# Kernel tuning notes

Hardware: AMD Instinct MI355X
Metric: run time of the kernel (lower is better)

The kernel has to match this reference:

```python
import jax, jax.numpy as jnp
import numpy as np

LOG_STD_MAX = 2.0
LOG_STD_MIN = -5.0
N_LAYERS = 10
HID = 512
OBS = 21
ACT = 8
OVERALL = HID * (N_LAYERS + 1)          # 5632
IN_DIM = OBS + OVERALL                   # 5653
OUT_DIM = OVERALL + ACT                  # 5640
BATCH = 8192


def _block_banded_weight(rng):
    # staircase partitions, exactly as layer_init
    in_d = [0, OBS] + [OBS + HID * i for i in range(1, N_LAYERS + 2)]
    out_d = [0] + [HID * i for i in range(1, N_LAYERS + 2)] + [OUT_DIM]
    W = np.zeros((OUT_DIM, IN_DIM), dtype=np.float32)
    for i in range(N_LAYERS + 2):
        r0, r1 = out_d[i], out_d[i + 1]
        c0, c1 = in_d[i], in_d[i + 1]
        fan_in = c1 - c0
        std = np.sqrt(2.0 / fan_in)  # kaiming_normal_ fan_in, gain sqrt(2)
        W[r0:r1, c0:c1] = rng.standard_normal((r1 - r0, c1 - c0)).astype(np.float32) * std
    return jnp.asarray(W)


def setup_inputs() -> dict:
    key = jax.random.key(0)
    k1, k2, k3, k4, k5, k6 = jax.random.split(key, 6)
    rng = np.random.default_rng(0)
    return {
        "obs": jax.random.normal(k1, (BATCH, OBS), dtype=jnp.float32),
        "hidden0": jax.random.uniform(k2, (BATCH, OVERALL), dtype=jnp.float32),
        "prev_mean": jax.random.normal(k3, (BATCH, ACT), dtype=jnp.float32),
        "prev_logstd": jax.random.normal(k4, (BATCH, ACT), dtype=jnp.float32),
        "W_mean": _block_banded_weight(rng),
        "b_mean": jnp.zeros((OUT_DIM,), dtype=jnp.float32),
        "W_logstd": jax.random.normal(k5, (ACT, IN_DIM), dtype=jnp.float32) / np.sqrt(IN_DIM),
        "b_logstd": jax.random.normal(k6, (ACT,), dtype=jnp.float32) * 0.01,
    }


def reference(obs, hidden0, prev_mean, prev_logstd, W_mean, b_mean, W_logstd, b_logstd):
    x = jnp.concatenate([obs, hidden0], axis=1)            # [B, IN_DIM]
    new_x = x @ W_mean.T + b_mean                          # [B, OUT_DIM]
    new_hidden = jax.nn.relu(new_x[:, :-ACT])              # [B, OVERALL]
    new_mean = new_x[:, -ACT:]                             # [B, ACT]
    new_log_std = x @ W_logstd.T + b_logstd                # [B, ACT]
    # outputs come from the PREVIOUS step's (mean, log_std)
    log_std = jnp.tanh(prev_logstd)
    log_std = LOG_STD_MIN + 0.5 * (LOG_STD_MAX - LOG_STD_MIN) * (log_std + 1.0)
    return (prev_mean, log_std, new_hidden, new_mean, new_log_std)
```

## Files before the change

### kernel.cpp

```cpp
#include <hip/hip_runtime.h>
#include <math.h>

typedef unsigned short u16;
typedef unsigned int u32;
typedef __attribute__((ext_vector_type(8))) short short8;
typedef __attribute__((ext_vector_type(4))) float float4v;

#define BATCH   8192
#define OBS     21
#define HID     512
#define NL      10
#define OVERALL 5632
#define IN_DIM  5653
#define ACT     8

#define O_PM   0
#define O_LS   65536
#define O_NH   131072
#define O_NM   (131072 + BATCH*OVERALL)
#define O_NLS  (O_NM + 65536)

#define WSP_TOTAL (10*512*512)
#define WSP_BYTES ((size_t)WSP_TOTAL * 2)

__device__ __forceinline__ u16 f2bf(float f) {
    u32 u = __float_as_uint(f);
    u32 r = (u + 0x7fffu + ((u >> 16) & 1u)) >> 16;
    return (u16)r;
}
__device__ __forceinline__ u32 pkbf(float a, float b) {
    return (u32)f2bf(a) | ((u32)f2bf(b) << 16);
}
__device__ __forceinline__ void gload_lds16(const void* g, void* l) {
    __builtin_amdgcn_global_load_lds(
        (const __attribute__((address_space(1))) char*)g,
        (__attribute__((address_space(3))) char*)l, 16, 0, 0);
}

__global__ __launch_bounds__(256) void k_pack(const float* __restrict__ Wm,
                                              u16* __restrict__ ws) {
    int idx4 = blockIdx.x * 256 + threadIdx.x;
    if (idx4 >= WSP_TOTAL / 4) return;
    int idx = idx4 * 4;
    int z = idx >> 18;
    int rem = idx & 262143;
    int n = rem >> 9, k = rem & 511;
    const float* g = Wm + (size_t)(512 * (z + 1) + n) * IN_DIM + OBS + 512 * z + k;
    ushort4 o;
    o.x = f2bf(g[0]); o.y = f2bf(g[1]); o.z = f2bf(g[2]); o.w = f2bf(g[3]);
    *(ushort4*)&ws[idx] = o;
}

#define BM 128
#define BK 32
#define LDA 40
__global__ __launch_bounds__(1024, 4) void k_fused(
        const float* __restrict__ X,
        const float* __restrict__ Wm_raw,
        const u16* __restrict__ Wp,
        const float* __restrict__ Wls_raw,
        const float* __restrict__ b_mean,
        float* __restrict__ out_h,
        float* __restrict__ out_ls,
        float* __restrict__ out_mean,
        int packed) {
    __shared__ __attribute__((aligned(16))) u16 As[BM * LDA];
    __shared__ __attribute__((aligned(16))) u16 Bs[512 * 32];
    __shared__ __attribute__((aligned(16))) u16 Wt[16 * 520];
    u16* Wt2 = (u16*)Bs;

    int t = threadIdx.x;
    int w = t >> 6, lane = t & 63;
    int quad = lane >> 4, r16 = lane & 15;
    int gm = blockIdx.x * BM;
    int z = blockIdx.y;
    bool mainz = (z < 10);
    int wm = (w >> 3) * 64;
    int wn = (w & 7) * 64;

    {
        int n = t >> 7;
        int k4 = (t & 127) * 4;
        const float* wr = Wls_raw + (size_t)n * IN_DIM + OBS + z * 512 + k4;
        u16* dst = &Wt[n * 520 + k4];
        dst[0] = f2bf(wr[0]); dst[1] = f2bf(wr[1]);
        dst[2] = f2bf(wr[2]); dst[3] = f2bf(wr[3]);
        if (!mainz) {
            const float* wr2 = Wm_raw + (size_t)(OVERALL + n) * IN_DIM + OBS + z * 512 + k4;
            u16* d2 = &Wt2[n * 520 + k4];
            d2[0] = f2bf(wr2[0]); d2[1] = f2bf(wr2[1]);
            d2[2] = f2bf(wr2[2]); d2[3] = f2bf(wr2[3]);
        }
    }

    int arow = t >> 3;
    int acol = (t & 7) * 4;
    const float* gA = X + (size_t)(gm + arow) * OVERALL + (size_t)z * 512 + acol;
    float4 areg = *(const float4*)(gA);

    float4v acc[4][4];
#pragma unroll
    for (int i = 0; i < 4; i++)
#pragma unroll
        for (int j = 0; j < 4; j++) acc[i][j] = (float4v)0.f;
    float4v accL = (float4v)0.f;

    for (int it = 0; it < 16; ++it) {
        int k0 = it * BK;
        __syncthreads();
        {
            uint2 p;
            p.x = pkbf(areg.x, areg.y);
            p.y = pkbf(areg.z, areg.w);
            *(uint2*)&As[arow * LDA + acol] = p;
        }
        if (mainz) {
            if (packed) {
#pragma unroll
                for (int i2 = 0; i2 < 2; ++i2) {
                    int base_row = i2 * 256 + w * 16;
                    int row = base_row + (lane >> 2);
                    int slot = lane & 3;
                    int j = (slot - row) & 3;
                    const u16* g = Wp + (size_t)z * 262144 + (size_t)row * 512 + k0 + j * 8;
                    gload_lds16(g, (char*)Bs + base_row * 64);
                }
            } else {
#pragma unroll
                for (int i2 = 0; i2 < 2; ++i2) {
                    int row = i2 * 256 + w * 16 + (lane >> 2);
                    int slot = lane & 3;
                    int j = (slot - row) & 3;
                    const float* g = Wm_raw + (size_t)(512 * (z + 1) + row) * IN_DIM
                                     + OBS + (size_t)z * 512 + k0 + j * 8;
                    uint4 q;
                    q.x = pkbf(g[0], g[1]); q.y = pkbf(g[2], g[3]);
                    q.z = pkbf(g[4], g[5]); q.w = pkbf(g[6], g[7]);
                    *(uint4*)&Bs[row * 32 + slot * 8] = q;
                }
            }
        }
        __syncthreads();
        if (it < 15) areg = *(const float4*)(gA + (it + 1) * BK);

        if (mainz) {
            short8 bfr[4];
#pragma unroll
            for (int j = 0; j < 4; j++) {
                int n = wn + j * 16 + r16;
                int s = (quad + n) & 3;
                bfr[j] = *(const short8*)&Bs[n * 32 + s * 8];
            }
#pragma unroll
            for (int i2 = 0; i2 < 4; i2++) {
                short8 af = *(const short8*)&As[(wm + i2 * 16 + r16) * LDA + quad * 8];
#pragma unroll
                for (int j = 0; j < 4; j++)
                    acc[i2][j] = __builtin_amdgcn_mfma_f32_16x16x32_bf16(af, bfr[j], acc[i2][j], 0, 0, 0);
            }
        }
        if (w < 8) {
            short8 aL = *(const short8*)&As[(w * 16 + r16) * LDA + quad * 8];
            short8 bL = *(const short8*)&Wt[r16 * 520 + k0 + quad * 8];
            accL = __builtin_amdgcn_mfma_f32_16x16x32_bf16(aL, bL, accL, 0, 0, 0);
        } else if (!mainz) {
            short8 aL = *(const short8*)&As[((w - 8) * 16 + r16) * LDA + quad * 8];
            short8 bL = *(const short8*)&Wt2[r16 * 520 + k0 + quad * 8];
            accL = __builtin_amdgcn_mfma_f32_16x16x32_bf16(aL, bL, accL, 0, 0, 0);
        }
    }

    if (mainz) {
        int colblock = (z + 1) * 512;
#pragma unroll
        for (int j = 0; j < 4; j++) {
            int n_loc = wn + j * 16 + r16;
            float bias = b_mean[colblock + n_loc];
#pragma unroll
            for (int i2 = 0; i2 < 4; i2++) {
                int m0 = gm + wm + i2 * 16 + quad * 4;
#pragma unroll
                for (int r = 0; r < 4; r++) {
                    float v = acc[i2][j][r] + bias;
                    out_h[(size_t)(m0 + r) * OVERALL + colblock + n_loc] = fmaxf(v, 0.f);
                }
            }
        }
    }
    if (w < 8) {
        if (r16 < ACT) {
#pragma unroll
            for (int r = 0; r < 4; r++) {
                int row = gm + w * 16 + quad * 4 + r;
                atomicAdd(&out_ls[(size_t)row * ACT + r16], accL[r]);
            }
        }
    } else if (!mainz) {
        if (r16 < ACT) {
            float bias = b_mean[OVERALL + r16];
#pragma unroll
            for (int r = 0; r < 4; r++) {
                int row = gm + (w - 8) * 16 + quad * 4 + r;
                out_mean[(size_t)row * ACT + r16] = accL[r] + bias;
            }
        }
    }
}

#define B0_ROWS 32
__global__ __launch_bounds__(256) void k_epi(const float* __restrict__ obs,
                                             const float* __restrict__ Wm,
                                             const float* __restrict__ b_mean,
                                             const float* __restrict__ Wls,
                                             const float* __restrict__ b_logstd,
                                             const float* __restrict__ pm,
                                             const float* __restrict__ pls,
                                             float* __restrict__ out_h,
                                             float* __restrict__ o_pm,
                                             float* __restrict__ o_lstd,
                                             float* __restrict__ o_nls) {
    __shared__ float w0[OBS * 512];
    __shared__ float bias_s[512];
    __shared__ float obs_s[B0_ROWS * OBS];
    __shared__ float wobs[ACT * OBS];
    __shared__ float bls_s[ACT];
    int t = threadIdx.x;
    int b0 = blockIdx.x * B0_ROWS;
    for (int i = t; i < OBS * 512; i += 256) {
        int n = i / OBS, k = i - n * OBS;
        w0[k * 512 + n] = Wm[(size_t)n * IN_DIM + k];
    }
    for (int i = t; i < 512; i += 256) bias_s[i] = b_mean[i];
    for (int i = t; i < B0_ROWS * OBS; i += 256) obs_s[i] = obs[(size_t)b0 * OBS + i];
    if (t < ACT * OBS) wobs[t] = Wls[(size_t)(t / OBS) * IN_DIM + (t % OBS)];
    if (t < ACT) bls_s[t] = b_logstd[t];
    __syncthreads();

    {
        int n0 = (t & 127) * 4;
        int rh = t >> 7;
#pragma unroll 4
        for (int r = 0; r < 16; r++) {
            int row = rh * 16 + r;
            float acc0 = bias_s[n0], acc1 = bias_s[n0 + 1];
            float acc2 = bias_s[n0 + 2], acc3 = bias_s[n0 + 3];
#pragma unroll
            for (int k = 0; k < OBS; k++) {
                float xo = obs_s[row * OBS + k];
                const float* wr = &w0[k * 512 + n0];
                acc0 += xo * wr[0]; acc1 += xo * wr[1];
                acc2 += xo * wr[2]; acc3 += xo * wr[3];
            }
            float4 o;
            o.x = fmaxf(acc0, 0.f); o.y = fmaxf(acc1, 0.f);
            o.z = fmaxf(acc2, 0.f); o.w = fmaxf(acc3, 0.f);
            *(float4*)&out_h[(size_t)(b0 + row) * OVERALL + n0] = o;
        }
    }

    {
        int rl = t >> 3;
        int n = t & 7;
        int row = b0 + rl;
        float a = bls_s[n];
#pragma unroll
        for (int k = 0; k < OBS; k++) a += obs_s[rl * OBS + k] * wobs[n * OBS + k];
        size_t off = (size_t)row * ACT + n;
        o_nls[off] += a;
        o_pm[off] = pm[off];
        float l = pls[off];
        o_lstd[off] = -5.f + 3.5f * (tanhf(l) + 1.f);
    }
}

extern "C" void kernel_launch(void* const* d_in, const int* in_sizes, int n_in,
                              void* d_out, int out_size, void* d_ws, size_t ws_size,
                              hipStream_t stream) {
    const float* obs         = (const float*)d_in[0];
    const float* hidden0     = (const float*)d_in[1];
    const float* prev_mean   = (const float*)d_in[2];
    const float* prev_logstd = (const float*)d_in[3];
    const float* W_mean      = (const float*)d_in[4];
    const float* b_mean      = (const float*)d_in[5];
    const float* W_logstd    = (const float*)d_in[6];
    const float* b_logstd    = (const float*)d_in[7];

    float* out   = (float*)d_out;
    float* o_pm  = out + O_PM;
    float* o_ls  = out + O_LS;
    float* o_nh  = out + O_NH;
    float* o_nm  = out + O_NM;
    float* o_nls = out + O_NLS;
    u16*   ws    = (u16*)d_ws;

    int packed = (ws != nullptr && ws_size >= WSP_BYTES) ? 1 : 0;

    if (packed) {
        k_pack<<<(WSP_TOTAL / 4 + 255) / 256, 256, 0, stream>>>(W_mean, ws);
    }
    hipMemsetAsync(o_nls, 0, (size_t)BATCH * ACT * sizeof(float), stream);
    k_fused<<<dim3(BATCH / BM, NL + 1), 1024, 0, stream>>>(
        hidden0, W_mean, ws, W_logstd, b_mean, o_nh, o_nls, o_nm, packed);
    k_epi<<<BATCH / B0_ROWS, 256, 0, stream>>>(obs, W_mean, b_mean,
                                               W_logstd, b_logstd,
                                               prev_mean, prev_logstd,
                                               o_nh, o_pm, o_ls, o_nls);
}
```

Baseline: 447.4 us.

## Make fused GEMM kernel persistent over 256 blocks with custom barriers

```diff
diff --git a/kernel.cpp b/kernel.cpp
--- a/kernel.cpp
+++ b/kernel.cpp
@@ -35,6 +35,14 @@
     __builtin_amdgcn_global_load_lds(
         (const __attribute__((address_space(1))) char*)g,
         (__attribute__((address_space(3))) char*)l, 16, 0, 0);
+}
+__device__ __forceinline__ void bar_lds() {
+    asm volatile("s_waitcnt lgkmcnt(0)" ::: "memory");
+    __builtin_amdgcn_s_barrier();
+}
+__device__ __forceinline__ void bar_full() {
+    asm volatile("s_waitcnt vmcnt(0) lgkmcnt(0)" ::: "memory");
+    __builtin_amdgcn_s_barrier();
 }
 
 __global__ __launch_bounds__(256) void k_pack(const float* __restrict__ Wm,
@@ -54,6 +62,7 @@
 #define BM 128
 #define BK 32
 #define LDA 40
+#define NTILES (64 * (NL + 1))
 __global__ __launch_bounds__(1024, 4) void k_fused(
         const float* __restrict__ X,
         const float* __restrict__ Wm_raw,
@@ -69,139 +78,145 @@
     __shared__ __attribute__((aligned(16))) u16 Wt[16 * 520];
     u16* Wt2 = (u16*)Bs;
 
-    int t = threadIdx.x;
-    int w = t >> 6, lane = t & 63;
-    int quad = lane >> 4, r16 = lane & 15;
-    int gm = blockIdx.x * BM;
-    int z = blockIdx.y;
-    bool mainz = (z < 10);
-    int wm = (w >> 3) * 64;
-    int wn = (w & 7) * 64;
-
-    {
-        int n = t >> 7;
-        int k4 = (t & 127) * 4;
-        const float* wr = Wls_raw + (size_t)n * IN_DIM + OBS + z * 512 + k4;
-        u16* dst = &Wt[n * 520 + k4];
-        dst[0] = f2bf(wr[0]); dst[1] = f2bf(wr[1]);
-        dst[2] = f2bf(wr[2]); dst[3] = f2bf(wr[3]);
-        if (!mainz) {
-            const float* wr2 = Wm_raw + (size_t)(OVERALL + n) * IN_DIM + OBS + z * 512 + k4;
-            u16* d2 = &Wt2[n * 520 + k4];
-            d2[0] = f2bf(wr2[0]); d2[1] = f2bf(wr2[1]);
-            d2[2] = f2bf(wr2[2]); d2[3] = f2bf(wr2[3]);
-        }
-    }
-
-    int arow = t >> 3;
-    int acol = (t & 7) * 4;
-    const float* gA = X + (size_t)(gm + arow) * OVERALL + (size_t)z * 512 + acol;
-    float4 areg = *(const float4*)(gA);
-
-    float4v acc[4][4];
-#pragma unroll
-    for (int i = 0; i < 4; i++)
-#pragma unroll
-        for (int j = 0; j < 4; j++) acc[i][j] = (float4v)0.f;
-    float4v accL = (float4v)0.f;
-
-    for (int it = 0; it < 16; ++it) {
-        int k0 = it * BK;
-        __syncthreads();
+    const int t = threadIdx.x;
+    const int w = t >> 6, lane = t & 63;
+    const int quad = lane >> 4, r16 = lane & 15;
+    const int wm = (w >> 3) * 64;
+    const int wn = (w & 7) * 64;
+    const int arow = t >> 3;
+    const int acol = (t & 7) * 4;
+
+#pragma unroll 1
+    for (int tile = blockIdx.x; tile < NTILES; tile += 256) {
+        const int gm = (tile & 63) * BM;
+        const int z = tile >> 6;
+        const bool mainz = (z < 10);
+
+        bar_lds();
+
         {
-            uint2 p;
-            p.x = pkbf(areg.x, areg.y);
-            p.y = pkbf(areg.z, areg.w);
-            *(uint2*)&As[arow * LDA + acol] = p;
-        }
+            int n = t >> 7;
+            int k4 = (t & 127) * 4;
+            const float* wr = Wls_raw + (size_t)n * IN_DIM + OBS + z * 512 + k4;
+            u16* dst = &Wt[n * 520 + k4];
+            dst[0] = f2bf(wr[0]); dst[1] = f2bf(wr[1]);
+            dst[2] = f2bf(wr[2]); dst[3] = f2bf(wr[3]);
+            if (!mainz) {
+                const float* wr2 = Wm_raw + (size_t)(OVERALL + n) * IN_DIM + OBS + z * 512 + k4;
+                u16* d2 = &Wt2[n * 520 + k4];
+                d2[0] = f2bf(wr2[0]); d2[1] = f2bf(wr2[1]);
+                d2[2] = f2bf(wr2[2]); d2[3] = f2bf(wr2[3]);
+            }
+        }
+
+        const float* gA = X + (size_t)(gm + arow) * OVERALL + (size_t)z * 512 + acol;
+        float4 areg = *(const float4*)(gA);
+
+        float4v acc[4][4];
+#pragma unroll
+        for (int i = 0; i < 4; i++)
+#pragma unroll
+            for (int j = 0; j < 4; j++) acc[i][j] = (float4v)0.f;
+        float4v accL = (float4v)0.f;
+
+        for (int it = 0; it < 16; ++it) {
+            int k0 = it * BK;
+            bar_lds();
+            {
+                uint2 p;
+                p.x = pkbf(areg.x, areg.y);
+                p.y = pkbf(areg.z, areg.w);
+                *(uint2*)&As[arow * LDA + acol] = p;
+            }
+            if (mainz) {
+                if (packed) {
+#pragma unroll
+                    for (int i2 = 0; i2 < 2; ++i2) {
+                        int base_row = i2 * 256 + w * 16;
+                        int row = base_row + (lane >> 2);
+                        int slot = lane & 3;
+                        int j = (slot - row) & 3;
+                        const u16* g = Wp + (size_t)z * 262144 + (size_t)row * 512 + k0 + j * 8;
+                        gload_lds16(g, (char*)Bs + base_row * 64);
+                    }
+                } else {
+#pragma unroll
+                    for (int i2 = 0; i2 < 2; ++i2) {
+                        int row = i2 * 256 + w * 16 + (lane >> 2);
+                        int slot = lane & 3;
+                        int j = (slot - row) & 3;
+                        const float* g = Wm_raw + (size_t)(512 * (z + 1) + row) * IN_DIM
+                                         + OBS + (size_t)z * 512 + k0 + j * 8;
+                        uint4 q;
+                        q.x = pkbf(g[0], g[1]); q.y = pkbf(g[2], g[3]);
+                        q.z = pkbf(g[4], g[5]); q.w = pkbf(g[6], g[7]);
+                        *(uint4*)&Bs[row * 32 + slot * 8] = q;
+                    }
+                }
+            }
+            bar_full();
+            if (it < 15) areg = *(const float4*)(gA + (it + 1) * BK);
+
+            if (mainz) {
+                short8 bfr[4];
+#pragma unroll
+                for (int j = 0; j < 4; j++) {
+                    int n = wn + j * 16 + r16;
+                    int s = (quad + n) & 3;
+                    bfr[j] = *(const short8*)&Bs[n * 32 + s * 8];
+                }
+#pragma unroll
+                for (int i2 = 0; i2 < 4; i2++) {
+                    short8 af = *(const short8*)&As[(wm + i2 * 16 + r16) * LDA + quad * 8];
+#pragma unroll
+                    for (int j = 0; j < 4; j++)
+                        acc[i2][j] = __builtin_amdgcn_mfma_f32_16x16x32_bf16(af, bfr[j], acc[i2][j], 0, 0, 0);
+                }
+            }
+            if (w < 8) {
+                short8 aL = *(const short8*)&As[(w * 16 + r16) * LDA + quad * 8];
+                short8 bL = *(const short8*)&Wt[r16 * 520 + k0 + quad * 8];
+                accL = __builtin_amdgcn_mfma_f32_16x16x32_bf16(aL, bL, accL, 0, 0, 0);
+            } else if (!mainz) {
+                short8 aL = *(const short8*)&As[((w - 8) * 16 + r16) * LDA + quad * 8];
+                short8 bL = *(const short8*)&Wt2[r16 * 520 + k0 + quad * 8];
+                accL = __builtin_amdgcn_mfma_f32_16x16x32_bf16(aL, bL, accL, 0, 0, 0);
+            }
+        }
+
         if (mainz) {
-            if (packed) {
-#pragma unroll
-                for (int i2 = 0; i2 < 2; ++i2) {
-                    int base_row = i2 * 256 + w * 16;
-                    int row = base_row + (lane >> 2);
-                    int slot = lane & 3;
-                    int j = (slot - row) & 3;
-                    const u16* g = Wp + (size_t)z * 262144 + (size_t)row * 512 + k0 + j * 8;
-                    gload_lds16(g, (char*)Bs + base_row * 64);
-                }
-            } else {
-#pragma unroll
-                for (int i2 = 0; i2 < 2; ++i2) {
-                    int row = i2 * 256 + w * 16 + (lane >> 2);
-                    int slot = lane & 3;
-                    int j = (slot - row) & 3;
-                    const float* g = Wm_raw + (size_t)(512 * (z + 1) + row) * IN_DIM
-                                     + OBS + (size_t)z * 512 + k0 + j * 8;
-                    uint4 q;
-                    q.x = pkbf(g[0], g[1]); q.y = pkbf(g[2], g[3]);
-                    q.z = pkbf(g[4], g[5]); q.w = pkbf(g[6], g[7]);
-                    *(uint4*)&Bs[row * 32 + slot * 8] = q;
-                }
-            }
-        }
-        __syncthreads();
-        if (it < 15) areg = *(const float4*)(gA + (it + 1) * BK);
-
-        if (mainz) {
-            short8 bfr[4];
+            int colblock = (z + 1) * 512;
 #pragma unroll
             for (int j = 0; j < 4; j++) {
-                int n = wn + j * 16 + r16;
-                int s = (quad + n) & 3;
-                bfr[j] = *(const short8*)&Bs[n * 32 + s * 8];
-            }
-#pragma unroll
-            for (int i2 = 0; i2 < 4; i2++) {
-                short8 af = *(const short8*)&As[(wm + i2 * 16 + r16) * LDA + quad * 8];
-#pragma unroll
-                for (int j = 0; j < 4; j++)
-                    acc[i2][j] = __builtin_amdgcn_mfma_f32_16x16x32_bf16(af, bfr[j], acc[i2][j], 0, 0, 0);
+                int n_loc = wn + j * 16 + r16;
+                float bias = b_mean[colblock + n_loc];
+#pragma unroll
+                for (int i2 = 0; i2 < 4; i2++) {
+                    int m0 = gm + wm + i2 * 16 + quad * 4;
+#pragma unroll
+                    for (int r = 0; r < 4; r++) {
+                        float v = acc[i2][j][r] + bias;
+                        out_h[(size_t)(m0 + r) * OVERALL + colblock + n_loc] = fmaxf(v, 0.f);
+                    }
+                }
             }
         }
         if (w < 8) {
-            short8 aL = *(const short8*)&As[(w * 16 + r16) * LDA + quad * 8];
-            short8 bL = *(const short8*)&Wt[r16 * 520 + k0 + quad * 8];
-            accL = __builtin_amdgcn_mfma_f32_16x16x32_bf16(aL, bL, accL, 0, 0, 0);
+            if (r16 < ACT) {
+#pragma unroll
+                for (int r = 0; r < 4; r++) {
+                    int row = gm + w * 16 + quad * 4 + r;
+                    atomicAdd(&out_ls[(size_t)row * ACT + r16], accL[r]);
+                }
+            }
         } else if (!mainz) {
-            short8 aL = *(const short8*)&As[((w - 8) * 16 + r16) * LDA + quad * 8];
-            short8 bL = *(const short8*)&Wt2[r16 * 520 + k0 + quad * 8];
-            accL = __builtin_amdgcn_mfma_f32_16x16x32_bf16(aL, bL, accL, 0, 0, 0);
-        }
-    }
-
-    if (mainz) {
-        int colblock = (z + 1) * 512;
-#pragma unroll
-        for (int j = 0; j < 4; j++) {
-            int n_loc = wn + j * 16 + r16;
-            float bias = b_mean[colblock + n_loc];
-#pragma unroll
-            for (int i2 = 0; i2 < 4; i2++) {
-                int m0 = gm + wm + i2 * 16 + quad * 4;
+            if (r16 < ACT) {
+                float bias = b_mean[OVERALL + r16];
 #pragma unroll
                 for (int r = 0; r < 4; r++) {
-                    float v = acc[i2][j][r] + bias;
-                    out_h[(size_t)(m0 + r) * OVERALL + colblock + n_loc] = fmaxf(v, 0.f);
-                }
-            }
-        }
-    }
-    if (w < 8) {
-        if (r16 < ACT) {
-#pragma unroll
-            for (int r = 0; r < 4; r++) {
-                int row = gm + w * 16 + quad * 4 + r;
-                atomicAdd(&out_ls[(size_t)row * ACT + r16], accL[r]);
-            }
-        }
-    } else if (!mainz) {
-        if (r16 < ACT) {
-            float bias = b_mean[OVERALL + r16];
-#pragma unroll
-            for (int r = 0; r < 4; r++) {
-                int row = gm + (w - 8) * 16 + quad * 4 + r;
-                out_mean[(size_t)row * ACT + r16] = accL[r] + bias;
+                    int row = gm + (w - 8) * 16 + quad * 4 + r;
+                    out_mean[(size_t)row * ACT + r16] = accL[r] + bias;
+                }
             }
         }
     }
@@ -299,7 +314,7 @@
         k_pack<<<(WSP_TOTAL / 4 + 255) / 256, 256, 0, stream>>>(W_mean, ws);
     }
     hipMemsetAsync(o_nls, 0, (size_t)BATCH * ACT * sizeof(float), stream);
-    k_fused<<<dim3(BATCH / BM, NL + 1), 1024, 0, stream>>>(
+    k_fused<<<256, 1024, 0, stream>>>(
         hidden0, W_mean, ws, W_logstd, b_mean, o_nh, o_nls, o_nm, packed);
     k_epi<<<BATCH / B0_ROWS, 256, 0, stream>>>(obs, W_mean, b_mean,
                                                W_logstd, b_logstd,
```

Result: slower. 470.1 us (+5.1%).
